# Kernel optimization log

Hardware: AMD Instinct MI355X
Metric: run time of the kernel (lower is better)

Reference implementation:

```python
import jax, jax.numpy as jnp
import numpy as np

# MxCorrelation (MXNet/FlowNet correlation) parameters
PAD = 4            # pad_size
K = 1              # kernel_size
MAXD = 4           # max_displacement
S1 = 1             # stride1 (output stride)
S2 = 1             # stride2 (displacement stride)


def setup_inputs() -> dict:
    key = jax.random.key(0)
    k1, k2 = jax.random.split(key)
    B, C, H, W = 8, 128, 128, 128
    input1 = jax.random.normal(k1, (B, C, H, W), dtype=jnp.float32)
    input2 = jax.random.normal(k2, (B, C, H, W), dtype=jnp.float32)
    return {"input1": input1, "input2": input2}


def _correlation(a, b):
    # a, b: [B, C, H, W]; returns [B, gw*gw, top_h, top_w]
    B, C, H, W = a.shape
    kr = (K - 1) // 2                       # kernel radius
    border = MAXD + kr                      # border in padded coords
    pa = jnp.pad(a, ((0, 0), (0, 0), (PAD, PAD), (PAD, PAD)))
    pb = jnp.pad(b, ((0, 0), (0, 0), (PAD, PAD), (PAD, PAD)))
    Hp, Wp = H + 2 * PAD, W + 2 * PAD
    th = -(-(Hp - 2 * border) // S1)        # top_height (ceil div)
    tw = -(-(Wp - 2 * border) // S1)        # top_width
    ngr = MAXD // S2                        # neighborhood grid radius
    gw = 2 * ngr + 1                        # grid width -> gw*gw out channels
    sumelems = jnp.float32(K * K * C)       # MXNet normalization

    out = []
    # channel order matches MXNet: row displacement p outer, col q inner
    for p in range(-ngr, ngr + 1):
        for q in range(-ngr, ngr + 1):
            s2p, s2q = p * S2, q * S2
            acc = jnp.zeros((B, th, tw), dtype=a.dtype)
            for dy in range(-kr, kr + 1):
                for dx in range(-kr, kr + 1):
                    A = pa[:, :, border + dy: border + dy + th * S1: S1,
                           border + dx: border + dx + tw * S1: S1]
                    Bm = pb[:, :, border + s2p + dy: border + s2p + dy + th * S1: S1,
                            border + s2q + dx: border + s2q + dx + tw * S1: S1]
                    acc = acc + jnp.sum(A * Bm, axis=1)  # reduce over channels
            out.append(acc / sumelems)
    return jnp.stack(out, axis=1)  # [B, gw*gw, th, tw]


def reference(input1, input2):
    return _correlation(input1, input2)
```

## Files before the change

### kernel.cpp

```cpp
#include <hip/hip_runtime.h>


typedef __fp16 h2 __attribute__((ext_vector_type(2)));

#define BW2 144

#if __has_builtin(__builtin_amdgcn_fdot2)
  #define FDOT2(a, b, c) __builtin_amdgcn_fdot2((a), (b), (c), false)
#else
  static __device__ inline float FDOT2(h2 a, h2 b, float c) {
      return c + (float)a.x * (float)b.x + (float)a.y * (float)b.y;
  }
#endif

static __device__ inline float pk2f(float lo, float hi) {
    h2 v = __builtin_amdgcn_cvt_pkrtz(lo, hi);
    return __builtin_bit_cast(float, v);
}
static __device__ inline h2 f2h2(float f) { return __builtin_bit_cast(h2, f); }

#define BARRIER() do {                                    \
    asm volatile("" ::: "memory");                        \
    asm volatile("s_waitcnt lgkmcnt(0)" ::: "memory");    \
    __builtin_amdgcn_s_barrier();                         \
    asm volatile("" ::: "memory");                        \
} while (0)

__global__ __launch_bounds__(192, 4)
void corr_kernel(const float* __restrict__ A, const float* __restrict__ B,
                 float* __restrict__ out)
{
    const int bidx = blockIdx.x;
    const int bb = bidx & 7;
    const int t2 = bidx >> 3;
    const int y  = t2 & 127;
    const int pg = t2 >> 7;

    const int tid  = threadIdx.x;
    const int wave = tid >> 6;
    const int lane = tid & 63;
    const int cs   = lane >> 5;
    const int x0   = (lane & 31) << 2;
    const int pr   = pg * 3 + wave;

    __shared__ h2 a_s[2][2][128];
    __shared__ h2 b_s[2][3][2][BW2];

    float acc[9][4];
    #pragma unroll
    for (int q = 0; q < 9; ++q)
        #pragma unroll
        for (int i = 0; i < 4; ++i) acc[q][i] = 0.f;

    const long plane = 128L * 128L;
    const float* Abase = A + (long)bb * 128 * plane + (long)y * 128;
    const float* Bbase = B + (long)bb * 128 * plane;

    const int i4  = (tid & 31) << 2;
    const int rp  = tid >> 5;
    const int brw = rp >> 1;
    const int bpp = rp & 1;
    const int bys = y + pg * 3 + brw - 4;
    const bool bval = (unsigned)bys < 128u;
    const float* Bsrc = Bbase + (long)bys * 128 + i4;

    const bool aact = tid < 64;
    const int app = (tid >> 5) & 1;

    float4 rb0[2], rb1[2], ra0[2], ra1[2];

#define LOADC(CHUNK, S) do {                                             \
    const int ch0_ = (CHUNK) << 2;                                       \
    if (bval) {                                                          \
        const int c0_ = ch0_ + (bpp << 1);                               \
        rb0[(S)] = *(const float4*)(Bsrc + (long)c0_ * plane);           \
        rb1[(S)] = *(const float4*)(Bsrc + (long)(c0_ + 1) * plane);     \
    }                                                                    \
    if (aact) {                                                          \
        const int c0_ = ch0_ + (app << 1);                               \
        ra0[(S)] = *(const float4*)(Abase + (long)c0_ * plane + i4);     \
        ra1[(S)] = *(const float4*)(Abase + (long)(c0_ + 1) * plane + i4);\
    }                                                                    \
} while (0)

#define STAGE(S) do {                                                    \
    if (bval) {                                                          \
        float4 w_;                                                       \
        w_.x = pk2f(rb0[(S)].x, rb1[(S)].x);                             \
        w_.y = pk2f(rb0[(S)].y, rb1[(S)].y);                             \
        w_.z = pk2f(rb0[(S)].z, rb1[(S)].z);                             \
        w_.w = pk2f(rb0[(S)].w, rb1[(S)].w);                             \
        *(float4*)&b_s[(S)][brw][bpp][4 + i4] = w_;       \
    }                                                                    \
    if (aact) {                                                          \
        float4 w_;                                                       \
        w_.x = pk2f(ra0[(S)].x, ra1[(S)].x);                             \
        w_.y = pk2f(ra0[(S)].y, ra1[(S)].y);                             \
        w_.z = pk2f(ra0[(S)].z, ra1[(S)].z);                             \
        w_.w = pk2f(ra0[(S)].w, ra1[(S)].w);                             \
        *(float4*)&a_s[(S)][app][i4] = w_;                               \
    }                                                                    \
} while (0)

#define BODY(K, S) do {                                                          \
    {                                                                            \
        const float4 av  = *(const float4*)&a_s[(S)][cs][x0];                    \
        const float4 b0v = *(const float4*)&b_s[(S)][wave][cs][x0];              \
        const float4 b1v = *(const float4*)&b_s[(S)][wave][cs][x0 + 4];          \
        const float4 b2v = *(const float4*)&b_s[(S)][wave][cs][x0 + 8];          \
        const h2 a2[4] = { f2h2(av.x), f2h2(av.y), f2h2(av.z), f2h2(av.w) };     \
        const h2 w[12] = { f2h2(b0v.x), f2h2(b0v.y), f2h2(b0v.z), f2h2(b0v.w),   \
                           f2h2(b1v.x), f2h2(b1v.y), f2h2(b1v.z), f2h2(b1v.w),   \
                           f2h2(b2v.x), f2h2(b2v.y), f2h2(b2v.z), f2h2(b2v.w) }; \
        _Pragma("unroll")                                                        \
        for (int q = 0; q < 9; ++q)                                              \
            _Pragma("unroll")                                                    \
            for (int i = 0; i < 4; ++i)                                          \
                acc[q][i] = FDOT2(a2[i], w[q + i], acc[q][i]);                   \
    }                                                                            \
    if ((K) + 1 < 32) STAGE((S) ^ 1);                                            \
    if ((K) + 3 < 32) LOADC((K) + 3, (S) ^ 1);                                   \
    BARRIER();                                                                   \
} while (0)

    LOADC(0, 0);
    LOADC(1, 1);

    {
        float4* pa = (float4*)&a_s[0][0][0];
        const int na = 2 * 2 * 128 / 4;
        for (int i = tid; i < na; i += 192) pa[i] = make_float4(0.f, 0.f, 0.f, 0.f);
        float4* pb = (float4*)&b_s[0][0][0][0];
        const int nb = 2 * 3 * 2 * BW2 / 4;
        for (int i = tid; i < nb; i += 192) pb[i] = make_float4(0.f, 0.f, 0.f, 0.f);
    }
    BARRIER();
    STAGE(0);
    LOADC(2, 0);
    BARRIER();

    for (int k = 0; k < 32; k += 2) {
        BODY(k, 0);
        BODY(k + 1, 1);
    }

#undef BODY
#undef STAGE
#undef LOADC

    #pragma unroll
    for (int q = 0; q < 9; ++q)
        #pragma unroll
        for (int i = 0; i < 4; ++i)
            acc[q][i] += __shfl_down(acc[q][i], 32);

    if (cs == 0) {
        const float scale = 1.0f / 128.0f;
        float* obase = out + (((long)bb * 81 + (long)pr * 9) * 128 + y) * 128 + x0;
        #pragma unroll
        for (int q = 0; q < 9; ++q) {
            const float4 v = make_float4(acc[q][0] * scale, acc[q][1] * scale,
                                         acc[q][2] * scale, acc[q][3] * scale);
            *(float4*)(obase + (long)q * plane) = v;
        }
    }
}

extern "C" void kernel_launch(void* const* d_in, const int* in_sizes, int n_in,
                              void* d_out, int out_size, void* d_ws, size_t ws_size,
                              hipStream_t stream) {
    const float* a = (const float*)d_in[0];
    const float* b = (const float*)d_in[1];
    float* out = (float*)d_out;
    hipLaunchKernelGGL(corr_kernel, dim3(3072), dim3(192), 0, stream, a, b, out);
}
```

Baseline: 212.9 us.

## Stage 16 channels per barrier instead of 4 to cut synchronization count

The shared-memory pipeline moves from 4-channel chunks (32 barriers) to 16-channel super-chunks (8 iterations), with each thread issuing more global loads per stage and the compute unrolled over four channel pairs per buffer. The aim is fewer barriers and more memory-level parallelism per thread. LDS use grows about fourfold and more registers hold in-flight loads, so launch bounds drop to 3 blocks per CU, which lowers occupancy. Load prefetch distance is also shorter, one stage ahead instead of two chunks.

```diff
diff --git a/kernel.cpp b/kernel.cpp
--- a/kernel.cpp
+++ b/kernel.cpp
@@ -19,14 +19,7 @@
 }
 static __device__ inline h2 f2h2(float f) { return __builtin_bit_cast(h2, f); }
 
-#define BARRIER() do {                                    \
-    asm volatile("" ::: "memory");                        \
-    asm volatile("s_waitcnt lgkmcnt(0)" ::: "memory");    \
-    __builtin_amdgcn_s_barrier();                         \
-    asm volatile("" ::: "memory");                        \
-} while (0)
-
-__global__ __launch_bounds__(192, 4)
+__global__ __launch_bounds__(192, 3)
 void corr_kernel(const float* __restrict__ A, const float* __restrict__ B,
                  float* __restrict__ out)
 {
@@ -43,8 +36,8 @@
     const int x0   = (lane & 31) << 2;
     const int pr   = pg * 3 + wave;
 
-    __shared__ h2 a_s[2][2][128];
-    __shared__ h2 b_s[2][3][2][BW2];
+    __shared__ h2 a_s[2][8][128];
+    __shared__ h2 b_s[2][3][8][BW2];
 
     float acc[9][4];
     #pragma unroll
@@ -56,58 +49,80 @@
     const float* Abase = A + (long)bb * 128 * plane + (long)y * 128;
     const float* Bbase = B + (long)bb * 128 * plane;
 
-    const int i4  = (tid & 31) << 2;
-    const int rp  = tid >> 5;
-    const int brw = rp >> 1;
-    const int bpp = rp & 1;
-    const int bys = y + pg * 3 + brw - 4;
-    const bool bval = (unsigned)bys < 128u;
-    const float* Bsrc = Bbase + (long)bys * 128 + i4;
+    const float* Bu[4]; int Boff[4]; bool Bv[4];
+    #pragma unroll
+    for (int i = 0; i < 4; ++i) {
+        const int u   = tid + 192 * i;
+        const int r   = u >> 8;
+        const int rem = u & 255;
+        const int pru = rem >> 5;
+        const int col = rem & 31;
+        const int bys = y + pg * 3 + r - 4;
+        Bv[i]  = (unsigned)bys < 128u;
+        Bu[i]  = Bbase + (long)(Bv[i] ? bys : 0) * 128 + col * 4
+                       + (long)(2 * pru) * plane;
+        Boff[i] = (r * 8 + pru) * BW2 + 4 + col * 4;
+    }
+    const bool aact = tid < 128;
+    const float* Au[2]; int Aoff[2];
+    #pragma unroll
+    for (int i = 0; i < 2; ++i) {
+        const int u   = (tid & 127) + 128 * i;
+        const int pru = u >> 5;
+        const int col = u & 31;
+        Au[i]  = Abase + col * 4 + (long)(2 * pru) * plane;
+        Aoff[i] = pru * 128 + col * 4;
+    }
 
-    const bool aact = tid < 64;
-    const int app = (tid >> 5) & 1;
+    float4 rb[4][2], ra[2][2];
 
-    float4 rb0[2], rb1[2], ra0[2], ra1[2];
-
-#define LOADC(CHUNK, S) do {                                             \
-    const int ch0_ = (CHUNK) << 2;                                       \
-    if (bval) {                                                          \
-        const int c0_ = ch0_ + (bpp << 1);                               \
-        rb0[(S)] = *(const float4*)(Bsrc + (long)c0_ * plane);           \
-        rb1[(S)] = *(const float4*)(Bsrc + (long)(c0_ + 1) * plane);     \
+#define LOADS(SC) do {                                                   \
+    const long choff_ = (long)((SC) << 4) * plane;                       \
+    _Pragma("unroll")                                                    \
+    for (int i = 0; i < 2; ++i) if (aact) {                              \
+        ra[i][0] = *(const float4*)(Au[i] + choff_);                     \
+        ra[i][1] = *(const float4*)(Au[i] + choff_ + plane);             \
     }                                                                    \
-    if (aact) {                                                          \
-        const int c0_ = ch0_ + (app << 1);                               \
-        ra0[(S)] = *(const float4*)(Abase + (long)c0_ * plane + i4);     \
-        ra1[(S)] = *(const float4*)(Abase + (long)(c0_ + 1) * plane + i4);\
+    _Pragma("unroll")                                                    \
+    for (int i = 0; i < 4; ++i) if (Bv[i]) {                             \
+        rb[i][0] = *(const float4*)(Bu[i] + choff_);                     \
+        rb[i][1] = *(const float4*)(Bu[i] + choff_ + plane);             \
     }                                                                    \
 } while (0)
 
-#define STAGE(S) do {                                                    \
-    if (bval) {                                                          \
+#define STAGES(BUF) do {                                                 \
+    h2* bb_ = &b_s[(BUF)][0][0][0];                                      \
+    _Pragma("unroll")                                                    \
+    for (int i = 0; i < 4; ++i) if (Bv[i]) {                             \
         float4 w_;                                                       \
-        w_.x = pk2f(rb0[(S)].x, rb1[(S)].x);                             \
-        w_.y = pk2f(rb0[(S)].y, rb1[(S)].y);                             \
-        w_.z = pk2f(rb0[(S)].z, rb1[(S)].z);                             \
-        w_.w = pk2f(rb0[(S)].w, rb1[(S)].w);                             \
-        *(float4*)&b_s[(S)][brw][bpp][4 + i4] = w_;       \
+        w_.x = pk2f(rb[i][0].x, rb[i][1].x);                             \
+        w_.y = pk2f(rb[i][0].y, rb[i][1].y);                             \
+        w_.z = pk2f(rb[i][0].z, rb[i][1].z);                             \
+        w_.w = pk2f(rb[i][0].w, rb[i][1].w);                             \
+        *(float4*)(bb_ + Boff[i]) = w_;                                  \
     }                                                                    \
     if (aact) {                                                          \
-        float4 w_;                                                       \
-        w_.x = pk2f(ra0[(S)].x, ra1[(S)].x);                             \
-        w_.y = pk2f(ra0[(S)].y, ra1[(S)].y);                             \
-        w_.z = pk2f(ra0[(S)].z, ra1[(S)].z);                             \
-        w_.w = pk2f(ra0[(S)].w, ra1[(S)].w);                             \
-        *(float4*)&a_s[(S)][app][i4] = w_;                               \
+        h2* aa_ = &a_s[(BUF)][0][0];                                     \
+        _Pragma("unroll")                                                \
+        for (int i = 0; i < 2; ++i) {                                    \
+            float4 w_;                                                   \
+            w_.x = pk2f(ra[i][0].x, ra[i][1].x);                         \
+            w_.y = pk2f(ra[i][0].y, ra[i][1].y);                         \
+            w_.z = pk2f(ra[i][0].z, ra[i][1].z);                         \
+            w_.w = pk2f(ra[i][0].w, ra[i][1].w);                         \
+            *(float4*)(aa_ + Aoff[i]) = w_;                              \
+        }                                                                \
     }                                                                    \
 } while (0)
 
-#define BODY(K, S) do {                                                          \
-    {                                                                            \
-        const float4 av  = *(const float4*)&a_s[(S)][cs][x0];                    \
-        const float4 b0v = *(const float4*)&b_s[(S)][wave][cs][x0];              \
-        const float4 b1v = *(const float4*)&b_s[(S)][wave][cs][x0 + 4];          \
-        const float4 b2v = *(const float4*)&b_s[(S)][wave][cs][x0 + 8];          \
+#define COMPUTE(BUF) do {                                                        \
+    _Pragma("unroll")                                                            \
+    for (int pp = 0; pp < 4; ++pp) {                                             \
+        const int pair_ = (pp << 1) | cs;                                        \
+        const float4 av  = *(const float4*)&a_s[(BUF)][pair_][x0];               \
+        const float4 b0v = *(const float4*)&b_s[(BUF)][wave][pair_][x0];         \
+        const float4 b1v = *(const float4*)&b_s[(BUF)][wave][pair_][x0 + 4];     \
+        const float4 b2v = *(const float4*)&b_s[(BUF)][wave][pair_][x0 + 8];     \
         const h2 a2[4] = { f2h2(av.x), f2h2(av.y), f2h2(av.z), f2h2(av.w) };     \
         const h2 w[12] = { f2h2(b0v.x), f2h2(b0v.y), f2h2(b0v.z), f2h2(b0v.w),   \
                            f2h2(b1v.x), f2h2(b1v.y), f2h2(b1v.z), f2h2(b1v.w),   \
@@ -118,35 +133,33 @@
             for (int i = 0; i < 4; ++i)                                          \
                 acc[q][i] = FDOT2(a2[i], w[q + i], acc[q][i]);                   \
     }                                                                            \
-    if ((K) + 1 < 32) STAGE((S) ^ 1);                                            \
-    if ((K) + 3 < 32) LOADC((K) + 3, (S) ^ 1);                                   \
-    BARRIER();                                                                   \
 } while (0)
 
-    LOADC(0, 0);
-    LOADC(1, 1);
-
+    LOADS(0);
     {
         float4* pa = (float4*)&a_s[0][0][0];
-        const int na = 2 * 2 * 128 / 4;
+        const int na = 2 * 8 * 128 / 4;
         for (int i = tid; i < na; i += 192) pa[i] = make_float4(0.f, 0.f, 0.f, 0.f);
         float4* pb = (float4*)&b_s[0][0][0][0];
-        const int nb = 2 * 3 * 2 * BW2 / 4;
+        const int nb = 2 * 3 * 8 * BW2 / 4;
         for (int i = tid; i < nb; i += 192) pb[i] = make_float4(0.f, 0.f, 0.f, 0.f);
     }
-    BARRIER();
-    STAGE(0);
-    LOADC(2, 0);
-    BARRIER();
+    __syncthreads();
+    STAGES(0);
+    __syncthreads();
 
-    for (int k = 0; k < 32; k += 2) {
-        BODY(k, 0);
-        BODY(k + 1, 1);
+    #pragma unroll
+    for (int k = 0; k < 7; ++k) {
+        LOADS(k + 1);
+        COMPUTE(k & 1);
+        STAGES((k + 1) & 1);
+        __syncthreads();
     }
+    COMPUTE(1);
 
-#undef BODY
-#undef STAGE
-#undef LOADC
+#undef COMPUTE
+#undef STAGES
+#undef LOADS
 
     #pragma unroll
     for (int q = 0; q < 9; ++q)
```

Result: slower. 734.6 us (+245.0%).
